# Optimization experiments

Hardware: AMD Instinct MI355X
Metric: run time of the kernel (lower is better)

The kernel has to match this reference:

```python
import jax, jax.numpy as jnp
import numpy as np

E, H, L = 512, 1024, 4
VS, VT = 32000, 32000
B, SS, TT = 64, 48, 48
PAD = 0


def _cell(x, h, c, Wih, Whh, bih, bhh):
    # torch.nn.LSTMCell math: gate order i, f, g, o
    g = x @ Wih.T + h @ Whh.T + bih + bhh
    i, f, gg, o = jnp.split(g, 4, axis=-1)
    c = jax.nn.sigmoid(f) * c + jax.nn.sigmoid(i) * jnp.tanh(gg)
    h = jax.nn.sigmoid(o) * jnp.tanh(c)
    return h, c


def setup_inputs() -> dict:
    key = jax.random.key(0)
    ks = jax.random.split(key, 14)
    s = 0.05
    d = {}
    d['src_tokens'] = jax.random.randint(ks[0], (SS, B), 0, VS, dtype=jnp.int32)
    d['tgt_tokens'] = jax.random.randint(ks[1], (TT, B), 0, VT, dtype=jnp.int32)
    d['src_emb'] = jax.random.normal(ks[2], (VS, E)) * s
    d['tgt_emb'] = jax.random.normal(ks[3], (VT, E)) * s
    d['enc_Wih0'] = jax.random.normal(ks[4], (4 * H, E)) * s
    d['enc_WihR'] = jax.random.normal(ks[5], (L - 1, 4 * H, H)) * s
    d['enc_Whh'] = jax.random.normal(ks[6], (L, 4 * H, H)) * s
    d['enc_bih'] = jnp.zeros((L, 4 * H))
    d['enc_bhh'] = jnp.zeros((L, 4 * H))
    d['dec_Wih0'] = jax.random.normal(ks[7], (4 * H, E + H)) * s
    d['dec_WihR'] = jax.random.normal(ks[8], (L - 1, 4 * H, H)) * s
    d['dec_Whh'] = jax.random.normal(ks[9], (L, 4 * H, H)) * s
    d['dec_bih'] = jnp.zeros((L, 4 * H))
    d['dec_bhh'] = jnp.zeros((L, 4 * H))
    d['att_vec_W'] = jax.random.normal(ks[10], (H, 2 * H)) * s
    d['readout_W'] = jax.random.normal(ks[11], (VT, H)) * s
    return d


def _forward(src_tokens, tgt_tokens, src_emb, tgt_emb, enc_Wih0, enc_WihR,
             enc_Whh, enc_bih, enc_bhh, dec_Wih0, dec_WihR, dec_Whh, dec_bih,
             dec_bhh, att_vec_W, readout_W):
    src_x = src_emb[src_tokens]                      # [SS, B, E]
    h0 = jnp.zeros((L, B, H), src_emb.dtype)
    c0 = jnp.zeros((L, B, H), src_emb.dtype)

    def enc_step(carry, x_t):
        h, c = carry
        inp = x_t
        hs, cs = [], []
        for l in range(L):
            Wih = enc_Wih0 if l == 0 else enc_WihR[l - 1]
            hn, cn = _cell(inp, h[l], c[l], Wih, enc_Whh[l], enc_bih[l], enc_bhh[l])
            hs.append(hn); cs.append(cn)
            inp = hn
        return (jnp.stack(hs), jnp.stack(cs)), inp

    (hT, cT), enc_out = jax.lax.scan(enc_step, (h0, c0), src_x)
    src_enc = enc_out.transpose(1, 0, 2)             # [B, SS, H]

    # decoder init: last encoder layer (h, c) copied to every decoder layer
    hd = jnp.tile(hT[-1][None], (L, 1, 1))
    cd = jnp.tile(cT[-1][None], (L, 1, 1))
    tgt_x = tgt_emb[tgt_tokens[:-1]]                 # [TT-1, B, E]
    att0 = jnp.zeros((B, H), src_emb.dtype)

    def dec_step(carry, y_t):
        h, c, att = carry
        inp = jnp.concatenate([y_t, att], axis=-1)   # input feeding
        hs, cs = [], []
        for l in range(L):
            Wih = dec_Wih0 if l == 0 else dec_WihR[l - 1]
            hn, cn = _cell(inp, h[l], c[l], Wih, dec_Whh[l], dec_bih[l], dec_bhh[l])
            hs.append(hn); cs.append(cn)
            inp = hn
        h_top = hs[-1]
        # global attention, 'dot' score (full-length seqs -> all-zero mask is a no-op)
        scores = jnp.einsum('bsh,bh->bs', src_enc, h_top)
        alpha = jax.nn.softmax(scores, axis=-1)
        ctx = jnp.einsum('bs,bsh->bh', alpha, src_enc)
        att_t = jnp.tanh(jnp.concatenate([h_top, ctx], axis=-1) @ att_vec_W.T)
        return (jnp.stack(hs), jnp.stack(cs), att_t), att_t

    _, att_ves = jax.lax.scan(dec_step, (hd, cd, att0), tgt_x)  # [TT-1, B, H]

    logp = jax.nn.log_softmax(att_ves @ readout_W.T, axis=-1)   # [TT-1, B, VT]
    gold = tgt_tokens[1:]
    gold_lp = jnp.take_along_axis(logp, gold[..., None], axis=-1)[..., 0]
    mask = (gold != PAD).astype(logp.dtype)
    return (gold_lp * mask).sum(axis=0)              # [B]


def reference(src_tokens, tgt_tokens, src_emb, tgt_emb, enc_Wih0, enc_WihR,
              enc_Whh, enc_bih, enc_bhh, dec_Wih0, dec_WihR, dec_Whh, dec_bih,
              dec_bhh, att_vec_W, readout_W):
    return _forward(src_tokens, tgt_tokens, src_emb, tgt_emb, enc_Wih0,
                    enc_WihR, enc_Whh, enc_bih, enc_bhh, dec_Wih0, dec_WihR,
                    dec_Whh, dec_bih, dec_bhh, att_vec_W, readout_W)
```

## Files before the change

kernel.cpp:

```cpp
#include <hip/hip_runtime.h>


typedef __attribute__((ext_vector_type(8))) short bf16x8;
typedef __attribute__((ext_vector_type(4))) float f32x4;

#define SMEM_BYTES 65536

__device__ __forceinline__ float bf2f(ushort u) {
  union { uint i; float f; } v; v.i = ((uint)u) << 16; return v.f;
}
__device__ __forceinline__ ushort f2bf(float x) {
  union { float f; uint i; } v; v.f = x;
  uint r = (v.i + 0x7fffu + ((v.i >> 16) & 1u)) >> 16;
  return (ushort)r;
}
__device__ __forceinline__ uint pack2(float x, float y) {
  return (uint)f2bf(x) | ((uint)f2bf(y) << 16);
}
__device__ __forceinline__ float sigm(float x) {
  return __fdividef(1.f, 1.f + __expf(-x));
}
__device__ __forceinline__ float tanhf_fast(float x) {
  const float e = __expf(2.f * x);
  return 1.f - __fdividef(2.f, e + 1.f);
}

__device__ __forceinline__ void gemm_term(
    const ushort* __restrict__ A, int lda,
    const ushort* __restrict__ W, int ldw,
    int K, int m0, int n0,
    f32x4 acc[4], char* s)
{
  char* sA0 = s;
  char* sB0 = s + 16384;
  char* sA1 = s + 32768;
  char* sB1 = s + 49152;
  const int tid = threadIdx.x;
  const int lane = tid & 63;
  const int w = tid >> 6;
  const int r0 = tid >> 3;
  const int cge = (tid & 7) << 3;
  const int soX = r0 * 128 + (((tid & 7) << 4) ^ ((r0 & 7) << 4));
  const ushort* Ar0 = A + (size_t)(m0 + r0) * lda + cge;
  const ushort* Ar1 = A + (size_t)(m0 + r0 + 32) * lda + cge;
  const ushort* Wr0 = W + (size_t)(n0 + r0) * ldw + cge;
  const ushort* Wr1 = W + (size_t)(n0 + r0 + 32) * ldw + cge;

  uint4 a0 = *reinterpret_cast<const uint4*>(Ar0);
  uint4 a1 = *reinterpret_cast<const uint4*>(Ar1);
  uint4 a2 = *reinterpret_cast<const uint4*>(Ar0 + 64);
  uint4 a3 = *reinterpret_cast<const uint4*>(Ar1 + 64);
  uint4 b0 = *reinterpret_cast<const uint4*>(Wr0);
  uint4 b1 = *reinterpret_cast<const uint4*>(Wr1);
  uint4 b2 = *reinterpret_cast<const uint4*>(Wr0 + 64);
  uint4 b3 = *reinterpret_cast<const uint4*>(Wr1 + 64);
  *reinterpret_cast<uint4*>(sA0 + soX) = a0;
  *reinterpret_cast<uint4*>(sA0 + 4096 + soX) = a1;
  *reinterpret_cast<uint4*>(sA0 + 8192 + soX) = a2;
  *reinterpret_cast<uint4*>(sA0 + 12288 + soX) = a3;
  *reinterpret_cast<uint4*>(sB0 + soX) = b0;
  *reinterpret_cast<uint4*>(sB0 + 4096 + soX) = b1;
  *reinterpret_cast<uint4*>(sB0 + 8192 + soX) = b2;
  *reinterpret_cast<uint4*>(sB0 + 12288 + soX) = b3;
  if (K > 128) {
    a0 = *reinterpret_cast<const uint4*>(Ar0 + 128);
    a1 = *reinterpret_cast<const uint4*>(Ar1 + 128);
    a2 = *reinterpret_cast<const uint4*>(Ar0 + 192);
    a3 = *reinterpret_cast<const uint4*>(Ar1 + 192);
    b0 = *reinterpret_cast<const uint4*>(Wr0 + 128);
    b1 = *reinterpret_cast<const uint4*>(Wr1 + 128);
    b2 = *reinterpret_cast<const uint4*>(Wr0 + 192);
    b3 = *reinterpret_cast<const uint4*>(Wr1 + 192);
  }
  const int axor = (lane & 7) << 4;
  const int arow = (w * 16 + (lane & 15)) * 128;
  const int brow = (lane & 15) * 128;
  const int kb0 = (lane >> 4) << 4;
  for (int kt = 0; kt < K; kt += 128) {
    char* cA = (kt & 128) ? sA1 : sA0;
    char* cB = (kt & 128) ? sB1 : sB0;
    char* nA = (kt & 128) ? sA0 : sA1;
    char* nB = (kt & 128) ? sB0 : sB1;
    __syncthreads();
    if (kt + 128 < K) {
      *reinterpret_cast<uint4*>(nA + soX) = a0;
      *reinterpret_cast<uint4*>(nA + 4096 + soX) = a1;
      *reinterpret_cast<uint4*>(nA + 8192 + soX) = a2;
      *reinterpret_cast<uint4*>(nA + 12288 + soX) = a3;
      *reinterpret_cast<uint4*>(nB + soX) = b0;
      *reinterpret_cast<uint4*>(nB + 4096 + soX) = b1;
      *reinterpret_cast<uint4*>(nB + 8192 + soX) = b2;
      *reinterpret_cast<uint4*>(nB + 12288 + soX) = b3;
      if (kt + 256 < K) {
        a0 = *reinterpret_cast<const uint4*>(Ar0 + kt + 256);
        a1 = *reinterpret_cast<const uint4*>(Ar1 + kt + 256);
        a2 = *reinterpret_cast<const uint4*>(Ar0 + kt + 320);
        a3 = *reinterpret_cast<const uint4*>(Ar1 + kt + 320);
        b0 = *reinterpret_cast<const uint4*>(Wr0 + kt + 256);
        b1 = *reinterpret_cast<const uint4*>(Wr1 + kt + 256);
        b2 = *reinterpret_cast<const uint4*>(Wr0 + kt + 320);
        b3 = *reinterpret_cast<const uint4*>(Wr1 + kt + 320);
      }
    }
#pragma unroll
    for (int ks = 0; ks < 4; ++ks) {
      const int sb = (ks >> 1) * 8192;
      const int kb = ((ks & 1) << 6) + kb0;
      bf16x8 af = *reinterpret_cast<const bf16x8*>(cA + sb + arow + (kb ^ axor));
#pragma unroll
      for (int nf = 0; nf < 4; ++nf) {
        bf16x8 bfr = *reinterpret_cast<const bf16x8*>(
            cB + sb + nf * 2048 + brow + (kb ^ axor));
        acc[nf] = __builtin_amdgcn_mfma_f32_16x16x32_bf16(af, bfr, acc[nf], 0, 0, 0);
      }
    }
  }
  __syncthreads();
}

__device__ __forceinline__ void att_loadf(
    const float* H0, const float* H1, const float* C0, const float* C1,
    int kt, float4* fh, float4* fc)
{
#pragma unroll
  for (int q = 0; q < 8; ++q) {
    const int rh = q >> 2, sub = (q >> 1) & 1, vq = q & 1;
    const float* hp_ = rh ? H1 : H0;
    const float* cp_ = rh ? C1 : C0;
    fh[q] = *reinterpret_cast<const float4*>(hp_ + kt + sub * 64 + vq * 4);
    fc[q] = *reinterpret_cast<const float4*>(cp_ + kt + sub * 64 + vq * 4);
  }
}

__device__ __forceinline__ void att_store(
    char* buf, int soX, const float4* fh, const float4* fc)
{
#pragma unroll
  for (int rh = 0; rh < 2; ++rh)
#pragma unroll
    for (int sub = 0; sub < 2; ++sub) {
      const int q0 = rh * 4 + sub * 2;
      const float4 u = fh[q0], v = fc[q0];
      const float4 u2 = fh[q0 + 1], v2 = fc[q0 + 1];
      uint4 o;
      o.x = pack2(tanhf_fast(u.x + v.x), tanhf_fast(u.y + v.y));
      o.y = pack2(tanhf_fast(u.z + v.z), tanhf_fast(u.w + v.w));
      o.z = pack2(tanhf_fast(u2.x + v2.x), tanhf_fast(u2.y + v2.y));
      o.w = pack2(tanhf_fast(u2.z + v2.z), tanhf_fast(u2.w + v2.w));
      *reinterpret_cast<uint4*>(buf + sub * 8192 + rh * 4096 + soX) = o;
    }
}

__device__ __forceinline__ void gemm_att(
    const float* __restrict__ H, const float* __restrict__ C2,
    const ushort* __restrict__ W, int ldw, int n0,
    f32x4 acc[4], char* s)
{
  char* sA0 = s;
  char* sB0 = s + 16384;
  char* sA1 = s + 32768;
  char* sB1 = s + 49152;
  const int tid = threadIdx.x;
  const int lane = tid & 63;
  const int w = tid >> 6;
  const int r0 = tid >> 3;
  const int cge = (tid & 7) << 3;
  const int soX = r0 * 128 + (((tid & 7) << 4) ^ ((r0 & 7) << 4));
  const ushort* Wr0 = W + (size_t)(n0 + r0) * ldw + cge;
  const ushort* Wr1 = W + (size_t)(n0 + r0 + 32) * ldw + cge;
  const float* H0 = H + r0 * 1024 + cge;
  const float* H1 = H + (r0 + 32) * 1024 + cge;
  const float* C0 = C2 + r0 * 1024 + cge;
  const float* C1 = C2 + (r0 + 32) * 1024 + cge;

  float4 fh[8], fc[8];
  uint4 b0, b1, b2, b3;
  att_loadf(H0, H1, C0, C1, 0, fh, fc);
  att_store(sA0, soX, fh, fc);
  b0 = *reinterpret_cast<const uint4*>(Wr0);
  b1 = *reinterpret_cast<const uint4*>(Wr1);
  b2 = *reinterpret_cast<const uint4*>(Wr0 + 64);
  b3 = *reinterpret_cast<const uint4*>(Wr1 + 64);
  *reinterpret_cast<uint4*>(sB0 + soX) = b0;
  *reinterpret_cast<uint4*>(sB0 + 4096 + soX) = b1;
  *reinterpret_cast<uint4*>(sB0 + 8192 + soX) = b2;
  *reinterpret_cast<uint4*>(sB0 + 12288 + soX) = b3;
  att_loadf(H0, H1, C0, C1, 128, fh, fc);
  b0 = *reinterpret_cast<const uint4*>(Wr0 + 128);
  b1 = *reinterpret_cast<const uint4*>(Wr1 + 128);
  b2 = *reinterpret_cast<const uint4*>(Wr0 + 192);
  b3 = *reinterpret_cast<const uint4*>(Wr1 + 192);

  const int axor = (lane & 7) << 4;
  const int arow = (w * 16 + (lane & 15)) * 128;
  const int brow = (lane & 15) * 128;
  const int kb0 = (lane >> 4) << 4;
  for (int kt = 0; kt < 1024; kt += 128) {
    char* cA = (kt & 128) ? sA1 : sA0;
    char* cB = (kt & 128) ? sB1 : sB0;
    char* nA = (kt & 128) ? sA0 : sA1;
    char* nB = (kt & 128) ? sB0 : sB1;
    __syncthreads();
    if (kt + 128 < 1024) {
      att_store(nA, soX, fh, fc);
      *reinterpret_cast<uint4*>(nB + soX) = b0;
      *reinterpret_cast<uint4*>(nB + 4096 + soX) = b1;
      *reinterpret_cast<uint4*>(nB + 8192 + soX) = b2;
      *reinterpret_cast<uint4*>(nB + 12288 + soX) = b3;
      if (kt + 256 < 1024) {
        att_loadf(H0, H1, C0, C1, kt + 256, fh, fc);
        b0 = *reinterpret_cast<const uint4*>(Wr0 + kt + 256);
        b1 = *reinterpret_cast<const uint4*>(Wr1 + kt + 256);
        b2 = *reinterpret_cast<const uint4*>(Wr0 + kt + 320);
        b3 = *reinterpret_cast<const uint4*>(Wr1 + kt + 320);
      }
    }
#pragma unroll
    for (int ks = 0; ks < 4; ++ks) {
      const int sb = (ks >> 1) * 8192;
      const int kb = ((ks & 1) << 6) + kb0;
      bf16x8 af = *reinterpret_cast<const bf16x8*>(cA + sb + arow + (kb ^ axor));
#pragma unroll
      for (int nf = 0; nf < 4; ++nf) {
        bf16x8 bfr = *reinterpret_cast<const bf16x8*>(
            cB + sb + nf * 2048 + brow + (kb ^ axor));
        acc[nf] = __builtin_amdgcn_mfma_f32_16x16x32_bf16(af, bfr, acc[nf], 0, 0, 0);
      }
    }
  }
  __syncthreads();
}

__device__ __forceinline__ void store_f32(
    float* __restrict__ out, int ldo, int m0, int n0, f32x4 acc[4])
{
  const int tid = threadIdx.x, lane = tid & 63, w = tid >> 6;
  const int rbase = w * 16 + ((lane >> 4) << 2);
  const int cb = lane & 15;
#pragma unroll
  for (int nf = 0; nf < 4; ++nf)
#pragma unroll
    for (int r = 0; r < 4; ++r)
      out[(size_t)(m0 + rbase + r) * ldo + n0 + nf * 16 + cb] = acc[nf][r];
}

__device__ __forceinline__ void cell_store(
    float* smemF, f32x4 acc[4],
    float* __restrict__ c, ushort* __restrict__ hout,
    ushort* __restrict__ senc_t, int j0)
{
  const int tid = threadIdx.x, lane = tid & 63, w = tid >> 6;
  const int rbase = w * 16 + ((lane >> 4) << 2);
  const int cb = lane & 15;
  __syncthreads();
#pragma unroll
  for (int nf = 0; nf < 4; ++nf)
#pragma unroll
    for (int r = 0; r < 4; ++r)
      smemF[(rbase + r) * 68 + nf * 16 + cb] = acc[nf][r];
  __syncthreads();
#pragma unroll
  for (int i = 0; i < 4; ++i) {
    const int id = tid + i * 256;
    const int b = id >> 4, u = id & 15;
    const float g0 = smemF[b * 68 + u * 4 + 0];
    const float g1 = smemF[b * 68 + u * 4 + 1];
    const float g2 = smemF[b * 68 + u * 4 + 2];
    const float g3 = smemF[b * 68 + u * 4 + 3];
    const int off = b * 1024 + j0 + u;
    const float cold = c[off];
    const float cn = sigm(g1) * cold + sigm(g0) * tanhf_fast(g2);
    const float hv = sigm(g3) * tanhf_fast(cn);
    c[off] = cn;
    const ushort hb = f2bf(hv);
    hout[off] = hb;
    if (senc_t) senc_t[(size_t)b * 49152 + j0 + u] = hb;
  }
}

__global__ __launch_bounds__(256) void nmt_init(
    float* c, ushort* henc, float* hbAll, float* ctxAll)
{
  const int idx = blockIdx.x * 256 + threadIdx.x;
  if (idx < 262144) c[idx] = 0.f;
  if (idx < 65536) {
    hbAll[idx] = 0.f;
    ctxAll[idx] = 0.f;
    henc[idx] = 0;
    henc[(size_t)1 * 49 * 65536 + idx] = 0;
    henc[(size_t)2 * 49 * 65536 + idx] = 0;
    henc[(size_t)3 * 49 * 65536 + idx] = 0;
  }
}

__global__ __launch_bounds__(256) void nmt_convperm(
    const float* __restrict__ in, ushort* __restrict__ out,
    int L, int Kin, int col0, int Kout)
{
  const size_t idx = (size_t)blockIdx.x * 256 + threadIdx.x;
  const size_t total = (size_t)L * 4096 * Kout;
  if (idx >= total) return;
  const int k = (int)(idx % Kout);
  const size_t rem = idx / Kout;
  const int rp = (int)(rem % 4096);
  const int l = (int)(rem / 4096);
  const int j = rp >> 2, g = rp & 3;
  out[idx] = f2bf(in[((size_t)l * 4096 + g * 1024 + j) * Kin + col0 + k]);
}

__global__ __launch_bounds__(256) void nmt_convplain(
    const float* __restrict__ in, ushort* __restrict__ out, size_t n)
{
  const size_t idx = (size_t)blockIdx.x * 256 + threadIdx.x;
  if (idx < n) out[idx] = f2bf(in[idx]);
}

__global__ __launch_bounds__(256) void nmt_bias(
    const float* __restrict__ bih, const float* __restrict__ bhh, float* __restrict__ bc)
{
  const int idx = blockIdx.x * 256 + threadIdx.x;
  if (idx >= 4 * 4096) return;
  const int rp = idx & 4095, l = idx >> 12;
  const int j = rp >> 2, g = rp & 3;
  bc[idx] = bih[l * 4096 + g * 1024 + j] + bhh[l * 4096 + g * 1024 + j];
}

__global__ __launch_bounds__(256) void nmt_gather(
    const int* __restrict__ tok, const float* __restrict__ emb,
    ushort* __restrict__ out, int rows)
{
  const size_t idx = (size_t)blockIdx.x * 256 + threadIdx.x;
  if (idx >= (size_t)rows * 512) return;
  const int k = (int)(idx & 511);
  const int r = (int)(idx >> 9);
  out[idx] = f2bf(emb[(size_t)tok[r] * 512 + k]);
}

__global__ __launch_bounds__(256) void nmt_pre(
    const ushort* __restrict__ A, const ushort* __restrict__ Wp,
    const float* __restrict__ bc0, float* __restrict__ out, int K)
{
  __shared__ __align__(16) char smem[SMEM_BYTES];
  const int m0 = blockIdx.x * 64, n0 = blockIdx.y * 64;
  const int lane = threadIdx.x & 63;
  const int cb = lane & 15;
  f32x4 acc[4];
#pragma unroll
  for (int nf = 0; nf < 4; ++nf) {
    const float bv = bc0[n0 + nf * 16 + cb];
#pragma unroll
    for (int r = 0; r < 4; ++r) acc[nf][r] = bv;
  }
  gemm_term(A, K, Wp, K, K, m0, n0, acc, smem);
  store_f32(out, 4096, m0, n0, acc);
}

__global__ __launch_bounds__(256) void nmt_decinit(
    const ushort* __restrict__ henc, float* c, ushort* h)
{
  const int idx = blockIdx.x * 256 + threadIdx.x;
  if (idx >= 65536) return;
  const ushort hv = henc[((size_t)3 * 49 + 48) * 65536 + idx];
  const float cv = c[3 * 65536 + idx];
  c[idx] = cv; c[65536 + idx] = cv; c[2 * 65536 + idx] = cv;
  h[idx] = hv; h[65536 + idx] = hv; h[2 * 65536 + idx] = hv; h[3 * 65536 + idx] = hv;
}

__global__ __launch_bounds__(256) void nmt_sv(
    const ushort* __restrict__ senc, const ushort* __restrict__ attW,
    ushort* __restrict__ SV)
{
  __shared__ __align__(16) char smem[SMEM_BYTES];
  const int b = blockIdx.x;
  const int n0 = blockIdx.y * 64;
  const int tid = threadIdx.x, lane = tid & 63, w = tid >> 6;
  const int rbase = w * 16 + ((lane >> 4) << 2), cb = lane & 15;
  f32x4 acc[4];
#pragma unroll
  for (int nf = 0; nf < 4; ++nf)
#pragma unroll
    for (int r = 0; r < 4; ++r) acc[nf][r] = 0.f;
  gemm_term(senc + (size_t)b * 49152, 1024, attW + 1024, 2048, 1024, 0, n0,
            acc, smem);
#pragma unroll
  for (int nf = 0; nf < 4; ++nf)
#pragma unroll
    for (int r = 0; r < 4; ++r) {
      const int row = rbase + r;
      if (row < 48)
        SV[(size_t)b * 49152 + row * 1024 + n0 + nf * 16 + cb] = f2bf(acc[nf][r]);
    }
}

__global__ __launch_bounds__(256) void nmt_enc_cell(
    int u, int lo, ushort* __restrict__ henc, ushort* __restrict__ srcenc,
    float* __restrict__ c,
    const ushort* __restrict__ WihR, const ushort* __restrict__ Whh,
    const float* __restrict__ X0, const float* __restrict__ bcE)
{
  __shared__ __align__(16) char smem[SMEM_BYTES];
  const int l = lo + blockIdx.y;
  const int t = u - l;
  const int n0 = blockIdx.x * 64;
  const int tid = threadIdx.x, lane = tid & 63, w = tid >> 6;
  const int rbase = w * 16 + ((lane >> 4) << 2), cb = lane & 15;
  f32x4 acc[4];
  if (l == 0) {
#pragma unroll
    for (int nf = 0; nf < 4; ++nf)
#pragma unroll
      for (int r = 0; r < 4; ++r)
        acc[nf][r] = X0[(size_t)t * 262144 + (size_t)(rbase + r) * 4096 + n0 + nf * 16 + cb];
  } else {
#pragma unroll
    for (int nf = 0; nf < 4; ++nf) {
      const float bv = bcE[l * 4096 + n0 + nf * 16 + cb];
#pragma unroll
      for (int r = 0; r < 4; ++r) acc[nf][r] = bv;
    }
    gemm_term(henc + ((size_t)(l - 1) * 49 + t + 1) * 65536, 1024,
              WihR + (size_t)(l - 1) * 4194304, 1024, 1024, 0, n0, acc, smem);
  }
  gemm_term(henc + ((size_t)l * 49 + t) * 65536, 1024,
            Whh + (size_t)l * 4194304, 1024, 1024, 0, n0, acc, smem);
  cell_store((float*)smem, acc, c + l * 65536,
             henc + ((size_t)l * 49 + t + 1) * 65536,
             (l == 3) ? (srcenc + t * 1024) : (ushort*)nullptr, n0 >> 2);
}

__global__ __launch_bounds__(256) void nmt_dec_stage(
    int l, const ushort* __restrict__ hp, ushort* __restrict__ hn,
    float* __restrict__ c,
    const ushort* __restrict__ Whh, const ushort* __restrict__ WihR,
    const ushort* __restrict__ Wd0a,
    const float* __restrict__ hbprev, const float* __restrict__ ctxprev,
    const float* __restrict__ Y0t, const float* __restrict__ bcD,
    float* __restrict__ pbuf)
{
  __shared__ __align__(16) char smem[SMEM_BYTES];
  const int n0 = blockIdx.x * 64;
  const int tid = threadIdx.x, lane = tid & 63, w = tid >> 6;
  const int rbase = w * 16 + ((lane >> 4) << 2), cb = lane & 15;
  f32x4 acc[4];
  if (blockIdx.y == 0) {
    if (l == 0) {
#pragma unroll
      for (int nf = 0; nf < 4; ++nf)
#pragma unroll
        for (int r = 0; r < 4; ++r) {
          const size_t o = (size_t)(rbase + r) * 4096 + n0 + nf * 16 + cb;
          acc[nf][r] = Y0t[o] + pbuf[o];
        }
      gemm_att(hbprev, ctxprev, Wd0a, 1024, n0, acc, smem);
    } else {
#pragma unroll
      for (int nf = 0; nf < 4; ++nf)
#pragma unroll
        for (int r = 0; r < 4; ++r)
          acc[nf][r] = pbuf[(size_t)l * 262144 + (size_t)(rbase + r) * 4096 + n0 + nf * 16 + cb];
      gemm_term(hn + (l - 1) * 65536, 1024, WihR + (size_t)(l - 1) * 4194304,
                1024, 1024, 0, n0, acc, smem);
    }
    cell_store((float*)smem, acc, c + l * 65536, hn + l * 65536,
               (ushort*)nullptr, n0 >> 2);
  } else {
    const int lp = (l + 1) & 3;
    if (lp == 0) {
#pragma unroll
      for (int nf = 0; nf < 4; ++nf)
#pragma unroll
        for (int r = 0; r < 4; ++r) acc[nf][r] = 0.f;
      gemm_term(hn, 1024, Whh, 1024, 1024, 0, n0, acc, smem);
    } else {
#pragma unroll
      for (int nf = 0; nf < 4; ++nf) {
        const float bv = bcD[lp * 4096 + n0 + nf * 16 + cb];
#pragma unroll
        for (int r = 0; r < 4; ++r) acc[nf][r] = bv;
      }
      gemm_term(hp + lp * 65536, 1024, Whh + (size_t)lp * 4194304,
                1024, 1024, 0, n0, acc, smem);
    }
    store_f32(pbuf + (size_t)lp * 262144, 4096, 0, n0, acc);
  }
}

__global__ __launch_bounds__(256) void nmt_partial0(
    const ushort* __restrict__ h0, const ushort* __restrict__ Whh0,
    float* __restrict__ pbuf)
{
  __shared__ __align__(16) char smem[SMEM_BYTES];
  const int n0 = blockIdx.x * 64;
  f32x4 acc[4];
#pragma unroll
  for (int nf = 0; nf < 4; ++nf)
#pragma unroll
    for (int r = 0; r < 4; ++r) acc[nf][r] = 0.f;
  gemm_term(h0, 1024, Whh0, 1024, 1024, 0, n0, acc, smem);
  store_f32(pbuf, 4096, 0, n0, acc);
}

__global__ __launch_bounds__(256) void nmt_attnAB(
    const ushort* __restrict__ h3, const ushort* __restrict__ senc,
    const ushort* __restrict__ SV, const ushort* __restrict__ attW,
    float* __restrict__ ctx2, float* __restrict__ hb)
{
  __shared__ __align__(16) char smem[SMEM_BYTES];
  const int bid = blockIdx.x;
  const int tid = threadIdx.x, lane = tid & 63, w = tid >> 6;
  if (bid < 64) {
    float* sc = (float*)smem;
    float* al = (float*)smem + 64;
    const int b = bid;
    const ushort* sb = senc + (size_t)b * 49152;
    const ushort* vb = SV + (size_t)b * 49152;
    float hreg[16];
#pragma unroll
    for (int q = 0; q < 16; ++q) hreg[q] = bf2f(h3[b * 1024 + lane * 16 + q]);
    for (int s = w; s < 48; s += 4) {
      const ushort* vr = sb + s * 1024 + lane * 16;
      float p = 0.f;
#pragma unroll
      for (int q = 0; q < 16; ++q) p += bf2f(vr[q]) * hreg[q];
      for (int d = 1; d < 64; d <<= 1) p += __shfl_xor(p, d);
      if (lane == 0) sc[s] = p;
    }
    __syncthreads();
    if (tid < 64) {
      const float v = (lane < 48) ? sc[lane] : -3.4e38f;
      float m = v;
      for (int d = 1; d < 64; d <<= 1) m = fmaxf(m, __shfl_xor(m, d));
      float e = (lane < 48) ? expf(v - m) : 0.f;
      float s = e;
      for (int d = 1; d < 64; d <<= 1) s += __shfl_xor(s, d);
      al[lane] = e / s;
    }
    __syncthreads();
    const int k0 = tid * 4;
    float a0 = 0, a1 = 0, a2 = 0, a3 = 0;
    for (int s = 0; s < 48; ++s) {
      const float als = al[s];
      const ushort* vr = vb + s * 1024 + k0;
      a0 += als * bf2f(vr[0]); a1 += als * bf2f(vr[1]);
      a2 += als * bf2f(vr[2]); a3 += als * bf2f(vr[3]);
    }
    ctx2[b * 1024 + k0 + 0] = a0; ctx2[b * 1024 + k0 + 1] = a1;
    ctx2[b * 1024 + k0 + 2] = a2; ctx2[b * 1024 + k0 + 3] = a3;
  } else {
    const int n0 = (bid - 64) * 64;
    f32x4 acc[4];
#pragma unroll
    for (int nf = 0; nf < 4; ++nf)
#pragma unroll
      for (int r = 0; r < 4; ++r) acc[nf][r] = 0.f;
    gemm_term(h3, 1024, attW, 2048, 1024, 0, n0, acc, smem);
    store_f32(hb, 1024, 0, n0, acc);
  }
}

__global__ __launch_bounds__(256) void nmt_attves_k(
    const float* __restrict__ hbAll, const float* __restrict__ ctxAll,
    ushort* __restrict__ attves)
{
  const int i = blockIdx.x * 1024 + threadIdx.x * 4;
#pragma unroll
  for (int k = 0; k < 4; ++k) {
    const int j = i + k;
    attves[j] = f2bf(tanhf_fast(hbAll[j + 65536] + ctxAll[j + 65536]));
  }
}

__global__ __launch_bounds__(256) void nmt_readout(
    const ushort* __restrict__ attves, const ushort* __restrict__ routW,
    const int* __restrict__ tgt, float* __restrict__ pmax,
    float* __restrict__ psum, float* __restrict__ goldl)
{
  __shared__ __align__(16) char smem[SMEM_BYTES];
  const int m0 = blockIdx.x * 64, n0 = blockIdx.y * 64;
  const int tid = threadIdx.x, lane = tid & 63, w = tid >> 6;
  const int rbase = w * 16 + ((lane >> 4) << 2), cb = lane & 15;
  f32x4 acc[4];
#pragma unroll
  for (int nf = 0; nf < 4; ++nf)
#pragma unroll
    for (int r = 0; r < 4; ++r) acc[nf][r] = 0.f;
  gemm_term(attves, 1024, routW, 1024, 1024, m0, n0, acc, smem);
#pragma unroll
  for (int r = 0; r < 4; ++r) {
    float lm = fmaxf(fmaxf(acc[0][r], acc[1][r]), fmaxf(acc[2][r], acc[3][r]));
    for (int d = 1; d < 16; d <<= 1) lm = fmaxf(lm, __shfl_xor(lm, d));
    float ls = 0.f;
#pragma unroll
    for (int nf = 0; nf < 4; ++nf) ls += expf(acc[nf][r] - lm);
    for (int d = 1; d < 16; d <<= 1) ls += __shfl_xor(ls, d);
    const int grow = m0 + rbase + r;
    if (cb == 0) {
      pmax[(size_t)grow * 500 + blockIdx.y] = lm;
      psum[(size_t)grow * 500 + blockIdx.y] = ls;
    }
    const int t = grow >> 6, b = grow & 63;
    const int gold = tgt[(t + 1) * 64 + b];
#pragma unroll
    for (int nf = 0; nf < 4; ++nf)
      if (n0 + nf * 16 + cb == gold) goldl[grow] = acc[nf][r];
  }
}

__global__ __launch_bounds__(64) void nmt_combine(
    const float* __restrict__ pmax, const float* __restrict__ psum,
    const float* __restrict__ goldl, const int* __restrict__ tgt,
    float* __restrict__ lpm)
{
  const int row = blockIdx.x;
  const int lane = threadIdx.x;
  float m = -3.4e38f, s = 0.f;
  for (int i = lane; i < 500; i += 64) {
    const float pm = pmax[(size_t)row * 500 + i];
    const float ps = psum[(size_t)row * 500 + i];
    if (pm > m) { s = s * expf(m - pm) + ps; m = pm; }
    else        { s += ps * expf(pm - m); }
  }
  for (int d = 1; d < 64; d <<= 1) {
    const float om = __shfl_xor(m, d), os = __shfl_xor(s, d);
    if (om > m) { s = s * expf(m - om) + os; m = om; }
    else        { s += os * expf(om - m); }
  }
  if (lane == 0) {
    const int t = row >> 6, b = row & 63;
    const int gold = tgt[(t + 1) * 64 + b];
    const float lp = goldl[row] - m - logf(s);
    lpm[row] = (gold != 0) ? lp : 0.f;
  }
}

__global__ __launch_bounds__(64) void nmt_final(
    const float* __restrict__ lpm, float* __restrict__ out)
{
  const int b = threadIdx.x;
  float s = 0.f;
  for (int t = 0; t < 47; ++t) s += lpm[t * 64 + b];
  out[b] = s;
}

extern "C" void kernel_launch(void* const* d_in, const int* in_sizes, int n_in,
                              void* d_out, int out_size, void* d_ws, size_t ws_size,
                              hipStream_t stream)
{
  (void)in_sizes; (void)n_in; (void)out_size; (void)ws_size;
  const int*   src_tok  = (const int*)d_in[0];
  const int*   tgt_tok  = (const int*)d_in[1];
  const float* src_emb  = (const float*)d_in[2];
  const float* tgt_emb  = (const float*)d_in[3];
  const float* eWih0    = (const float*)d_in[4];
  const float* eWihR    = (const float*)d_in[5];
  const float* eWhh     = (const float*)d_in[6];
  const float* ebih     = (const float*)d_in[7];
  const float* ebhh     = (const float*)d_in[8];
  const float* dWih0    = (const float*)d_in[9];
  const float* dWihR    = (const float*)d_in[10];
  const float* dWhh     = (const float*)d_in[11];
  const float* dbih     = (const float*)d_in[12];
  const float* dbhh     = (const float*)d_in[13];
  const float* attW_f   = (const float*)d_in[14];
  const float* routW_f  = (const float*)d_in[15];

  char* p = (char*)d_ws;
  auto alloc = [&](size_t bytes) { void* r = (void*)p; p += (bytes + 255) & ~(size_t)255; return r; };
  ushort* eWih0p = (ushort*)alloc((size_t)4096 * 512 * 2);
  ushort* eWihRp = (ushort*)alloc((size_t)3 * 4096 * 1024 * 2);
  ushort* eWhhp  = (ushort*)alloc((size_t)4 * 4096 * 1024 * 2);
  ushort* dWih0y = (ushort*)alloc((size_t)4096 * 512 * 2);
  ushort* dWih0a = (ushort*)alloc((size_t)4096 * 1024 * 2);
  ushort* dWihRp = (ushort*)alloc((size_t)3 * 4096 * 1024 * 2);
  ushort* dWhhp  = (ushort*)alloc((size_t)4 * 4096 * 1024 * 2);
  ushort* attWb  = (ushort*)alloc((size_t)1024 * 2048 * 2);
  ushort* routWb = (ushort*)alloc((size_t)32000 * 1024 * 2);
  ushort* srcx   = (ushort*)alloc((size_t)3072 * 512 * 2);
  ushort* tgtx   = (ushort*)alloc((size_t)3008 * 512 * 2);
  ushort* henc   = (ushort*)alloc((size_t)4 * 49 * 65536 * 2);
  ushort* hA     = (ushort*)alloc((size_t)4 * 65536 * 2);
  ushort* hB     = (ushort*)alloc((size_t)4 * 65536 * 2);
  ushort* srcenc = (ushort*)alloc((size_t)64 * 49152 * 2);
  ushort* SVbuf  = (ushort*)alloc((size_t)64 * 49152 * 2);
  ushort* attves = (ushort*)alloc((size_t)3008 * 1024 * 2);
  float*  hbAll  = (float*)alloc((size_t)48 * 65536 * 4);
  float*  ctxAll = (float*)alloc((size_t)48 * 65536 * 4);
  float*  pbuf   = (float*)alloc((size_t)4 * 262144 * 4);
  float*  X0     = (float*)alloc((size_t)3072 * 4096 * 4);
  float*  Y0     = (float*)alloc((size_t)3008 * 4096 * 4);
  float*  bcE    = (float*)alloc((size_t)16384 * 4);
  float*  bcD    = (float*)alloc((size_t)16384 * 4);
  float*  cbuf   = (float*)alloc((size_t)4 * 65536 * 4);
  float*  pmaxb  = (float*)alloc((size_t)3008 * 500 * 4);
  float*  psumb  = (float*)alloc((size_t)3008 * 500 * 4);
  float*  goldl  = (float*)alloc((size_t)3008 * 4);
  float*  lpm    = (float*)alloc((size_t)3008 * 4);

  const dim3 B256(256);
  auto g1 = [](size_t n) { return dim3((unsigned)((n + 255) / 256)); };

  nmt_init<<<g1(262144), B256, 0, stream>>>(cbuf, henc, hbAll, ctxAll);

  nmt_convperm<<<g1((size_t)4096 * 512), B256, 0, stream>>>(eWih0, eWih0p, 1, 512, 0, 512);
  nmt_convperm<<<g1((size_t)3 * 4096 * 1024), B256, 0, stream>>>(eWihR, eWihRp, 3, 1024, 0, 1024);
  nmt_convperm<<<g1((size_t)4 * 4096 * 1024), B256, 0, stream>>>(eWhh, eWhhp, 4, 1024, 0, 1024);
  nmt_convperm<<<g1((size_t)4096 * 512), B256, 0, stream>>>(dWih0, dWih0y, 1, 1536, 0, 512);
  nmt_convperm<<<g1((size_t)4096 * 1024), B256, 0, stream>>>(dWih0, dWih0a, 1, 1536, 512, 1024);
  nmt_convperm<<<g1((size_t)3 * 4096 * 1024), B256, 0, stream>>>(dWihR, dWihRp, 3, 1024, 0, 1024);
  nmt_convperm<<<g1((size_t)4 * 4096 * 1024), B256, 0, stream>>>(dWhh, dWhhp, 4, 1024, 0, 1024);
  nmt_convplain<<<g1((size_t)1024 * 2048), B256, 0, stream>>>(attW_f, attWb, (size_t)1024 * 2048);
  nmt_convplain<<<g1((size_t)32000 * 1024), B256, 0, stream>>>(routW_f, routWb, (size_t)32000 * 1024);
  nmt_bias<<<g1(16384), B256, 0, stream>>>(ebih, ebhh, bcE);
  nmt_bias<<<g1(16384), B256, 0, stream>>>(dbih, dbhh, bcD);
  nmt_gather<<<g1((size_t)3072 * 512), B256, 0, stream>>>(src_tok, src_emb, srcx, 3072);
  nmt_gather<<<g1((size_t)3008 * 512), B256, 0, stream>>>(tgt_tok, tgt_emb, tgtx, 3008);

  nmt_pre<<<dim3(48, 64), B256, 0, stream>>>(srcx, eWih0p, bcE, X0, 512);
  nmt_pre<<<dim3(47, 64), B256, 0, stream>>>(tgtx, dWih0y, bcD, Y0, 512);

  for (int u = 0; u < 51; ++u) {
    const int lo = (u > 47) ? (u - 47) : 0;
    const int hi = (u < 3) ? u : 3;
    nmt_enc_cell<<<dim3(64, hi - lo + 1), B256, 0, stream>>>(
        u, lo, henc, srcenc, cbuf, eWihRp, eWhhp, X0, bcE);
  }
  nmt_decinit<<<g1(65536), B256, 0, stream>>>(henc, cbuf, hA);
  nmt_sv<<<dim3(64, 16), B256, 0, stream>>>(srcenc, attWb, SVbuf);
  nmt_partial0<<<dim3(64), B256, 0, stream>>>(hA, dWhhp, pbuf);

  for (int t = 0; t < 47; ++t) {
    ushort* hp = (t & 1) ? hB : hA;
    ushort* hn = (t & 1) ? hA : hB;
    for (int l = 0; l < 4; ++l) {
      nmt_dec_stage<<<dim3(64, 2), B256, 0, stream>>>(
          l, hp, hn, cbuf, dWhhp, dWihRp, dWih0a,
          hbAll + (size_t)t * 65536, ctxAll + (size_t)t * 65536,
          Y0 + (size_t)t * 262144, bcD, pbuf);
    }
    nmt_attnAB<<<dim3(80), B256, 0, stream>>>(
        hn + 3 * 65536, srcenc, SVbuf, attWb,
        ctxAll + (size_t)(t + 1) * 65536, hbAll + (size_t)(t + 1) * 65536);
  }
  nmt_attves_k<<<dim3(3008), B256, 0, stream>>>(hbAll, ctxAll, attves);

  nmt_readout<<<dim3(47, 500), B256, 0, stream>>>(attves, routWb, tgt_tok,
                                                  pmaxb, psumb, goldl);
  nmt_combine<<<dim3(3008), dim3(64), 0, stream>>>(pmaxb, psumb, goldl, tgt_tok, lpm);
  nmt_final<<<dim3(1), dim3(64), 0, stream>>>(lpm, (float*)d_out);
}
```

Measured before the change: 4.499 ms.

## Restructure GEMM K-loop into triple-buffered 64-wide stages with deeper prefetch

The shared GEMM helper now uses 64-wide K tiles in three rotating shared-memory stages with register prefetch running further ahead, replacing the double-buffered 128-wide tiles. This halves the per-stage footprint, so most kernels shrink their shared allocation from 64KB to 48KB, which may allow more resident blocks per CU and better latency hiding. In exchange it issues twice as many barriers per K and adds more prefetch registers. The attention-decoder kernel keeps 64KB because it uses extra shared space.

```diff
diff --git a/kernel.cpp b/kernel.cpp
--- a/kernel.cpp
+++ b/kernel.cpp
@@ -4,7 +4,8 @@
 typedef __attribute__((ext_vector_type(8))) short bf16x8;
 typedef __attribute__((ext_vector_type(4))) float f32x4;
 
-#define SMEM_BYTES 65536
+#define SMEM_G  49152
+#define SMEM_A  65536
 
 __device__ __forceinline__ float bf2f(ushort u) {
   union { uint i; float f; } v; v.i = ((uint)u) << 16; return v.f;
@@ -31,90 +32,88 @@
     int K, int m0, int n0,
     f32x4 acc[4], char* s)
 {
-  char* sA0 = s;
-  char* sB0 = s + 16384;
-  char* sA1 = s + 32768;
-  char* sB1 = s + 49152;
   const int tid = threadIdx.x;
   const int lane = tid & 63;
   const int w = tid >> 6;
   const int r0 = tid >> 3;
   const int cge = (tid & 7) << 3;
-  const int soX = r0 * 128 + (((tid & 7) << 4) ^ ((r0 & 7) << 4));
+  const int so0 = r0 * 128 + (((tid & 7) << 4) ^ ((r0 & 7) << 4));
   const ushort* Ar0 = A + (size_t)(m0 + r0) * lda + cge;
   const ushort* Ar1 = A + (size_t)(m0 + r0 + 32) * lda + cge;
   const ushort* Wr0 = W + (size_t)(n0 + r0) * ldw + cge;
   const ushort* Wr1 = W + (size_t)(n0 + r0 + 32) * ldw + cge;
-
-  uint4 a0 = *reinterpret_cast<const uint4*>(Ar0);
-  uint4 a1 = *reinterpret_cast<const uint4*>(Ar1);
-  uint4 a2 = *reinterpret_cast<const uint4*>(Ar0 + 64);
-  uint4 a3 = *reinterpret_cast<const uint4*>(Ar1 + 64);
-  uint4 b0 = *reinterpret_cast<const uint4*>(Wr0);
-  uint4 b1 = *reinterpret_cast<const uint4*>(Wr1);
-  uint4 b2 = *reinterpret_cast<const uint4*>(Wr0 + 64);
-  uint4 b3 = *reinterpret_cast<const uint4*>(Wr1 + 64);
-  *reinterpret_cast<uint4*>(sA0 + soX) = a0;
-  *reinterpret_cast<uint4*>(sA0 + 4096 + soX) = a1;
-  *reinterpret_cast<uint4*>(sA0 + 8192 + soX) = a2;
-  *reinterpret_cast<uint4*>(sA0 + 12288 + soX) = a3;
-  *reinterpret_cast<uint4*>(sB0 + soX) = b0;
-  *reinterpret_cast<uint4*>(sB0 + 4096 + soX) = b1;
-  *reinterpret_cast<uint4*>(sB0 + 8192 + soX) = b2;
-  *reinterpret_cast<uint4*>(sB0 + 12288 + soX) = b3;
-  if (K > 128) {
-    a0 = *reinterpret_cast<const uint4*>(Ar0 + 128);
-    a1 = *reinterpret_cast<const uint4*>(Ar1 + 128);
-    a2 = *reinterpret_cast<const uint4*>(Ar0 + 192);
-    a3 = *reinterpret_cast<const uint4*>(Ar1 + 192);
-    b0 = *reinterpret_cast<const uint4*>(Wr0 + 128);
-    b1 = *reinterpret_cast<const uint4*>(Wr1 + 128);
-    b2 = *reinterpret_cast<const uint4*>(Wr0 + 192);
-    b3 = *reinterpret_cast<const uint4*>(Wr1 + 192);
-  }
+  const int NT = K >> 6;
+
+  uint4 a0s0, a1s0, b0s0, b1s0;
+  uint4 a0s1, a1s1, b0s1, b1s1;
+  uint4 a0s2, a1s2, b0s2, b1s2;
+
+  a0s0 = *(const uint4*)(Ar0);       a1s0 = *(const uint4*)(Ar1);
+  b0s0 = *(const uint4*)(Wr0);       b1s0 = *(const uint4*)(Wr1);
+  a0s1 = *(const uint4*)(Ar0 + 64);  a1s1 = *(const uint4*)(Ar1 + 64);
+  b0s1 = *(const uint4*)(Wr0 + 64);  b1s1 = *(const uint4*)(Wr1 + 64);
+  a0s2 = *(const uint4*)(Ar0 + 128); a1s2 = *(const uint4*)(Ar1 + 128);
+  b0s2 = *(const uint4*)(Wr0 + 128); b1s2 = *(const uint4*)(Wr1 + 128);
+  {
+    char* sl = s;
+    *(uint4*)(sl + so0) = a0s0;         *(uint4*)(sl + 4096 + so0) = a1s0;
+    *(uint4*)(sl + 8192 + so0) = b0s0;  *(uint4*)(sl + 12288 + so0) = b1s0;
+    sl = s + 16384;
+    *(uint4*)(sl + so0) = a0s1;         *(uint4*)(sl + 4096 + so0) = a1s1;
+    *(uint4*)(sl + 8192 + so0) = b0s1;  *(uint4*)(sl + 12288 + so0) = b1s1;
+  }
+  if (3 < NT) {
+    a0s0 = *(const uint4*)(Ar0 + 192); a1s0 = *(const uint4*)(Ar1 + 192);
+    b0s0 = *(const uint4*)(Wr0 + 192); b1s0 = *(const uint4*)(Wr1 + 192);
+  }
+  if (4 < NT) {
+    a0s1 = *(const uint4*)(Ar0 + 256); a1s1 = *(const uint4*)(Ar1 + 256);
+    b0s1 = *(const uint4*)(Wr0 + 256); b1s1 = *(const uint4*)(Wr1 + 256);
+  }
+
   const int axor = (lane & 7) << 4;
   const int arow = (w * 16 + (lane & 15)) * 128;
   const int brow = (lane & 15) * 128;
   const int kb0 = (lane >> 4) << 4;
-  for (int kt = 0; kt < K; kt += 128) {
-    char* cA = (kt & 128) ? sA1 : sA0;
-    char* cB = (kt & 128) ? sB1 : sB0;
-    char* nA = (kt & 128) ? sA0 : sA1;
-    char* nB = (kt & 128) ? sB0 : sB1;
-    __syncthreads();
-    if (kt + 128 < K) {
-      *reinterpret_cast<uint4*>(nA + soX) = a0;
-      *reinterpret_cast<uint4*>(nA + 4096 + soX) = a1;
-      *reinterpret_cast<uint4*>(nA + 8192 + soX) = a2;
-      *reinterpret_cast<uint4*>(nA + 12288 + soX) = a3;
-      *reinterpret_cast<uint4*>(nB + soX) = b0;
-      *reinterpret_cast<uint4*>(nB + 4096 + soX) = b1;
-      *reinterpret_cast<uint4*>(nB + 8192 + soX) = b2;
-      *reinterpret_cast<uint4*>(nB + 12288 + soX) = b3;
-      if (kt + 256 < K) {
-        a0 = *reinterpret_cast<const uint4*>(Ar0 + kt + 256);
-        a1 = *reinterpret_cast<const uint4*>(Ar1 + kt + 256);
-        a2 = *reinterpret_cast<const uint4*>(Ar0 + kt + 320);
-        a3 = *reinterpret_cast<const uint4*>(Ar1 + kt + 320);
-        b0 = *reinterpret_cast<const uint4*>(Wr0 + kt + 256);
-        b1 = *reinterpret_cast<const uint4*>(Wr1 + kt + 256);
-        b2 = *reinterpret_cast<const uint4*>(Wr0 + kt + 320);
-        b3 = *reinterpret_cast<const uint4*>(Wr1 + kt + 320);
-      }
-    }
-#pragma unroll
-    for (int ks = 0; ks < 4; ++ks) {
-      const int sb = (ks >> 1) * 8192;
-      const int kb = ((ks & 1) << 6) + kb0;
-      bf16x8 af = *reinterpret_cast<const bf16x8*>(cA + sb + arow + (kb ^ axor));
-#pragma unroll
-      for (int nf = 0; nf < 4; ++nf) {
-        bf16x8 bfr = *reinterpret_cast<const bf16x8*>(
-            cB + sb + nf * 2048 + brow + (kb ^ axor));
-        acc[nf] = __builtin_amdgcn_mfma_f32_16x16x32_bf16(af, bfr, acc[nf], 0, 0, 0);
-      }
-    }
-  }
+
+#define NMT_ROUND(KR, CUR, ST)                                                \
+  do {                                                                        \
+    __syncthreads();                                                          \
+    if ((KR) + 2 < NT) {                                                      \
+      char* sl_ = s + (ST) * 16384;                                           \
+      *(uint4*)(sl_ + so0) = a0s##ST;                                         \
+      *(uint4*)(sl_ + 4096 + so0) = a1s##ST;                                  \
+      *(uint4*)(sl_ + 8192 + so0) = b0s##ST;                                  \
+      *(uint4*)(sl_ + 12288 + so0) = b1s##ST;                                 \
+      if ((KR) + 5 < NT) {                                                    \
+        const int off_ = ((KR) + 5) << 6;                                     \
+        a0s##ST = *(const uint4*)(Ar0 + off_);                                \
+        a1s##ST = *(const uint4*)(Ar1 + off_);                                \
+        b0s##ST = *(const uint4*)(Wr0 + off_);                                \
+        b1s##ST = *(const uint4*)(Wr1 + off_);                                \
+      }                                                                       \
+    }                                                                         \
+    char* cur_ = s + (CUR) * 16384;                                           \
+    _Pragma("unroll")                                                         \
+    for (int ks = 0; ks < 2; ++ks) {                                          \
+      const int kb = (ks << 6) + kb0;                                         \
+      bf16x8 af = *(const bf16x8*)(cur_ + arow + (kb ^ axor));                \
+      _Pragma("unroll")                                                       \
+      for (int nf = 0; nf < 4; ++nf) {                                        \
+        bf16x8 bfr = *(const bf16x8*)(cur_ + 8192 + nf * 2048 + brow +        \
+                                      (kb ^ axor));                           \
+        acc[nf] = __builtin_amdgcn_mfma_f32_16x16x32_bf16(af, bfr, acc[nf],   \
+                                                          0, 0, 0);           \
+      }                                                                       \
+    }                                                                         \
+  } while (0)
+
+  for (int kb_ = 0; kb_ < NT; kb_ += 3) {
+    NMT_ROUND(kb_ + 0, 0, 2);
+    if (kb_ + 1 < NT) NMT_ROUND(kb_ + 1, 1, 0);
+    if (kb_ + 2 < NT) NMT_ROUND(kb_ + 2, 2, 1);
+  }
+#undef NMT_ROUND
   __syncthreads();
 }
 
@@ -340,7 +339,7 @@
     const ushort* __restrict__ A, const ushort* __restrict__ Wp,
     const float* __restrict__ bc0, float* __restrict__ out, int K)
 {
-  __shared__ __align__(16) char smem[SMEM_BYTES];
+  __shared__ __align__(16) char smem[SMEM_G];
   const int m0 = blockIdx.x * 64, n0 = blockIdx.y * 64;
   const int lane = threadIdx.x & 63;
   const int cb = lane & 15;
@@ -370,7 +369,7 @@
     const ushort* __restrict__ senc, const ushort* __restrict__ attW,
     ushort* __restrict__ SV)
 {
-  __shared__ __align__(16) char smem[SMEM_BYTES];
+  __shared__ __align__(16) char smem[SMEM_G];
   const int b = blockIdx.x;
   const int n0 = blockIdx.y * 64;
   const int tid = threadIdx.x, lane = tid & 63, w = tid >> 6;
@@ -398,7 +397,7 @@
     const ushort* __restrict__ WihR, const ushort* __restrict__ Whh,
     const float* __restrict__ X0, const float* __restrict__ bcE)
 {
-  __shared__ __align__(16) char smem[SMEM_BYTES];
+  __shared__ __align__(16) char smem[SMEM_G];
   const int l = lo + blockIdx.y;
   const int t = u - l;
   const int n0 = blockIdx.x * 64;
@@ -437,7 +436,7 @@
     const float* __restrict__ Y0t, const float* __restrict__ bcD,
     float* __restrict__ pbuf)
 {
-  __shared__ __align__(16) char smem[SMEM_BYTES];
+  __shared__ __align__(16) char smem[SMEM_A];
   const int n0 = blockIdx.x * 64;
   const int tid = threadIdx.x, lane = tid & 63, w = tid >> 6;
   const int rbase = w * 16 + ((lane >> 4) << 2), cb = lane & 15;
@@ -489,7 +488,7 @@
     const ushort* __restrict__ h0, const ushort* __restrict__ Whh0,
     float* __restrict__ pbuf)
 {
-  __shared__ __align__(16) char smem[SMEM_BYTES];
+  __shared__ __align__(16) char smem[SMEM_G];
   const int n0 = blockIdx.x * 64;
   f32x4 acc[4];
 #pragma unroll
@@ -505,7 +504,7 @@
     const ushort* __restrict__ SV, const ushort* __restrict__ attW,
     float* __restrict__ ctx2, float* __restrict__ hb)
 {
-  __shared__ __align__(16) char smem[SMEM_BYTES];
+  __shared__ __align__(16) char smem[SMEM_G];
   const int bid = blockIdx.x;
   const int tid = threadIdx.x, lane = tid & 63, w = tid >> 6;
   if (bid < 64) {
@@ -575,7 +574,7 @@
     const int* __restrict__ tgt, float* __restrict__ pmax,
     float* __restrict__ psum, float* __restrict__ goldl)
 {
-  __shared__ __align__(16) char smem[SMEM_BYTES];
+  __shared__ __align__(16) char smem[SMEM_G];
   const int m0 = blockIdx.x * 64, n0 = blockIdx.y * 64;
   const int tid = threadIdx.x, lane = tid & 63, w = tid >> 6;
   const int rbase = w * 16 + ((lane >> 4) << 2), cb = lane & 15;
```

Result: no change. 4.470 ms (-0.7%).
